# Performance work log

Hardware: AMD Instinct MI355X
Metric: run time of the kernel (lower is better)

The kernel has to match this reference:

```python
import jax, jax.numpy as jnp
import numpy as np

NEG_BIG = -9.0e15

def setup_inputs() -> dict:
    key = jax.random.key(0)
    k1, k2, k3, k4 = jax.random.split(key, 4)
    N, F_in, F_out = 2048, 512, 64
    x = jax.random.normal(k1, (N, F_in), dtype=jnp.float32)
    adj = jax.random.randint(k2, (N, N), 0, 2, dtype=jnp.int32)
    # xavier_uniform with gain=1.414
    def xavier(k, shape, gain=1.414):
        fan_in, fan_out = shape[0], shape[1]
        bound = gain * np.sqrt(6.0 / (fan_in + fan_out))
        return jax.random.uniform(k, shape, jnp.float32, -bound, bound)
    W = xavier(k3, (F_in, F_out))
    a = xavier(k4, (F_out, 1))
    return {"x": x, "adj": adj, "W": W, "a": a}

def reference(x, adj, W, a):
    h = x @ W                                  # [N, F_out]
    # pairwise |h_i - h_j| projected by a: e[i,j] = relu(sum_f |h_i,f - h_j,f| * a_f)
    diff = jnp.abs(h[:, None, :] - h[None, :, :])   # [N, N, F_out]
    e = jax.nn.relu(jnp.einsum('ijf,fo->ij', diff, a))  # [N, N]
    scores = jnp.where(adj > 0, e, NEG_BIG)
    attention = jax.nn.softmax(scores, axis=1)
    out = attention @ h                        # [N, F_out]
    return jax.nn.relu(out)                    # concat=True path
```

## Files before the change

kernel.cpp:

```cpp
#include <hip/hip_runtime.h>

#define Nn 2048
#define FIN 512
#define FO 64
#define SHIFT 20.0f
#define NJT 32
#define HS 68
#define PBS2 72
#define ZTOT (Nn * FO + Nn)

#define HX(r, f) ((r) * HS + ((((f) >> 2) ^ (((r) >> 2) & 15)) << 2))
#define HJX(r, f)  ((r) * PBS2 + ((((f) >> 3) ^ (((r) >> 2) & 7)) << 3) + ((f) & 7))
#define PX16(j, i) ((j) * PBS2 + ((((i) >> 3) ^ ((j) & 7)) << 3) + ((i) & 7))

__device__ __forceinline__ unsigned pk2(float x, float y) {
    unsigned r;
    asm("v_cvt_pk_bf16_f32 %0, %1, %2" : "=v"(r) : "v"(x), "v"(y));
    return r;
}
__device__ __forceinline__ float bflo(unsigned u) { return __uint_as_float(u << 16); }
__device__ __forceinline__ float bfhi(unsigned u) { return __uint_as_float(u & 0xffff0000u); }

__global__ __launch_bounds__(256) void gat_xw(const float* __restrict__ x,
                                              const float* __restrict__ W,
                                              float* __restrict__ h,
                                              float* __restrict__ z) {
    const int gt = blockIdx.x * 256 + threadIdx.x;
    if (z != nullptr && gt < ZTOT) z[gt] = 0.f;

    __shared__ float part[2][2][FO];
    const int wave = threadIdx.x >> 6;
    const int lane = threadIdx.x & 63;
    const int rs = wave >> 1;
    const int kh = wave & 1;
    int row = blockIdx.x * 2 + rs;
    row = __builtin_amdgcn_readfirstlane(row);
    const float* xr = x + (size_t)row * FIN + kh * (FIN / 2);
    const float* Wp = W + (size_t)kh * (FIN / 2) * FO;
    float acc = 0.f;
#pragma unroll 2
    for (int k = 0; k < FIN / 2; k += 8) {
        float4 xa = *(const float4*)(xr + k);
        float4 xb = *(const float4*)(xr + k + 4);
        acc = fmaf(xa.x, Wp[(k + 0) * FO + lane], acc);
        acc = fmaf(xa.y, Wp[(k + 1) * FO + lane], acc);
        acc = fmaf(xa.z, Wp[(k + 2) * FO + lane], acc);
        acc = fmaf(xa.w, Wp[(k + 3) * FO + lane], acc);
        acc = fmaf(xb.x, Wp[(k + 4) * FO + lane], acc);
        acc = fmaf(xb.y, Wp[(k + 5) * FO + lane], acc);
        acc = fmaf(xb.z, Wp[(k + 6) * FO + lane], acc);
        acc = fmaf(xb.w, Wp[(k + 7) * FO + lane], acc);
    }
    part[rs][kh][lane] = acc;
    __syncthreads();
    if (threadIdx.x < 128) {
        const int r2 = threadIdx.x >> 6;
        const int l2 = threadIdx.x & 63;
        h[((size_t)blockIdx.x * 2 + r2) * FO + l2] = part[r2][0][l2] + part[r2][1][l2];
    }
}

template <bool ATOMIC>
__global__ __launch_bounds__(256, 5) void gat_attn11(const float* __restrict__ h,
                                                     const int* __restrict__ adj,
                                                     const float* __restrict__ a,
                                                     float* __restrict__ po,
                                                     float* __restrict__ pl) {
    __shared__ __align__(16) float hi_s[64 * HS];
    __shared__ __align__(16) short hj16[64 * PBS2];
    __shared__ float a_s[FO];
    short* pT16 = (short*)hi_s;

    const int tid = threadIdx.x;
    const int w = tid >> 6;
    const int lane = tid & 63;
    const int li = lane & 3;
    const int lj = lane >> 2;
    const int it = blockIdx.x >> 5;
    const int jt = blockIdx.x & (NJT - 1);
    const int ib = it * 64;
    const int jb = jt * 64;
    const int iw = w * 16;

    for (int g4 = tid; g4 < 1024; g4 += 256) {
        const int row = g4 >> 4;
        const int f0 = (g4 & 15) * 4;
        *(float4*)&hi_s[HX(row, f0)] = *(const float4*)(h + (size_t)ib * FO + (size_t)g4 * 4);
        const float4 u = *(const float4*)(h + (size_t)jb * FO + (size_t)g4 * 4);
        uint2 pk;
        pk.x = pk2(u.x, u.y);
        pk.y = pk2(u.z, u.w);
        *(uint2*)&hj16[HJX(row, f0)] = pk;
    }
    if (tid < FO) a_s[tid] = a[tid];
    __syncthreads();

    float e[4][4];
#pragma unroll
    for (int di = 0; di < 4; di++)
#pragma unroll
        for (int dj = 0; dj < 4; dj++) e[di][dj] = 0.f;

#pragma unroll 4
    for (int f4 = 0; f4 < 16; f4++) {
        const float4 av = *(const float4*)&a_s[f4 * 4];
        float4 hi4[4], hj4[4];
#pragma unroll
        for (int d = 0; d < 4; d++) {
            hi4[d] = *(const float4*)&hi_s[HX(iw + 4 * li + d, f4 * 4)];
            const uint2 hw = *(const uint2*)&hj16[HJX(4 * lj + d, f4 * 4)];
            hj4[d].x = bflo(hw.x); hj4[d].y = bfhi(hw.x);
            hj4[d].z = bflo(hw.y); hj4[d].w = bfhi(hw.y);
        }
#pragma unroll
        for (int di = 0; di < 4; di++)
#pragma unroll
            for (int dj = 0; dj < 4; dj++) {
                e[di][dj] = fmaf(fabsf(hi4[di].x - hj4[dj].x), av.x, e[di][dj]);
                e[di][dj] = fmaf(fabsf(hi4[di].y - hj4[dj].y), av.y, e[di][dj]);
                e[di][dj] = fmaf(fabsf(hi4[di].z - hj4[dj].z), av.z, e[di][dj]);
                e[di][dj] = fmaf(fabsf(hi4[di].w - hj4[dj].w), av.w, e[di][dj]);
            }
    }

    float ls[4];
#pragma unroll
    for (int di = 0; di < 4; di++) ls[di] = 0.f;
#pragma unroll
    for (int di = 0; di < 4; di++) {
        const int4 am = *(const int4*)(adj + (size_t)(ib + iw + 4 * li + di) * Nn + (jb + 4 * lj));
        const int* ap = (const int*)&am;
#pragma unroll
        for (int dj = 0; dj < 4; dj++) {
            const float p = (ap[dj] > 0) ? __expf(fmaxf(e[di][dj], 0.f) - SHIFT) : 0.f;
            e[di][dj] = p;
            ls[di] += p;
        }
    }

    __syncthreads();

#pragma unroll
    for (int dj = 0; dj < 4; dj++) {
        uint2 pk;
        pk.x = pk2(e[0][dj], e[1][dj]);
        pk.y = pk2(e[2][dj], e[3][dj]);
        *(uint2*)&pT16[PX16(4 * lj + dj, iw + 4 * li)] = pk;
    }

    float pv[4][4];
#pragma unroll
    for (int u = 0; u < 4; u++)
#pragma unroll
        for (int v2 = 0; v2 < 4; v2++) pv[u][v2] = 0.f;

#pragma unroll 4
    for (int j = 0; j < 64; j++) {
        const uint2 pw = *(const uint2*)&pT16[PX16(j, iw + 4 * li)];
        const uint2 hw = *(const uint2*)&hj16[HJX(j, 4 * lj)];
        const float p0 = bflo(pw.x), p1 = bfhi(pw.x), p2 = bflo(pw.y), p3 = bfhi(pw.y);
        const float h0 = bflo(hw.x), h1 = bfhi(hw.x), h2 = bflo(hw.y), h3 = bfhi(hw.y);
        pv[0][0] = fmaf(p0, h0, pv[0][0]); pv[0][1] = fmaf(p0, h1, pv[0][1]);
        pv[0][2] = fmaf(p0, h2, pv[0][2]); pv[0][3] = fmaf(p0, h3, pv[0][3]);
        pv[1][0] = fmaf(p1, h0, pv[1][0]); pv[1][1] = fmaf(p1, h1, pv[1][1]);
        pv[1][2] = fmaf(p1, h2, pv[1][2]); pv[1][3] = fmaf(p1, h3, pv[1][3]);
        pv[2][0] = fmaf(p2, h0, pv[2][0]); pv[2][1] = fmaf(p2, h1, pv[2][1]);
        pv[2][2] = fmaf(p2, h2, pv[2][2]); pv[2][3] = fmaf(p2, h3, pv[2][3]);
        pv[3][0] = fmaf(p3, h0, pv[3][0]); pv[3][1] = fmaf(p3, h1, pv[3][1]);
        pv[3][2] = fmaf(p3, h2, pv[3][2]); pv[3][3] = fmaf(p3, h3, pv[3][3]);
    }

#pragma unroll
    for (int di = 0; di < 4; di++) {
        float v = ls[di];
        v += __shfl_xor(v, 4, 64);
        v += __shfl_xor(v, 8, 64);
        v += __shfl_xor(v, 16, 64);
        v += __shfl_xor(v, 32, 64);
        ls[di] = v;
    }

    if constexpr (!ATOMIC) {
        if (lj == 0) {
#pragma unroll
            for (int di = 0; di < 4; di++)
                pl[(size_t)jt * Nn + (ib + iw + 4 * li + di)] = ls[di];
        }
#pragma unroll
        for (int di = 0; di < 4; di++)
            *(float4*)&po[((size_t)jt * Nn + (ib + iw + 4 * li + di)) * FO + 4 * lj] =
                make_float4(pv[di][0], pv[di][1], pv[di][2], pv[di][3]);
    } else {
        if (lj == 0) {
#pragma unroll
            for (int di = 0; di < 4; di++)
                atomicAdd(&pl[ib + iw + 4 * li + di], ls[di]);
        }
#pragma unroll
        for (int di = 0; di < 4; di++) {
#pragma unroll
            for (int v2 = 0; v2 < 4; v2++)
                atomicAdd(&po[(size_t)(ib + iw + 4 * li + di) * FO + 4 * lj + v2], pv[di][v2]);
        }
    }
}

__global__ __launch_bounds__(256) void gat_reduce(const float* __restrict__ po,
                                                  const float* __restrict__ pl,
                                                  float* __restrict__ out) {
    const int t = blockIdx.x * 256 + threadIdx.x;
    const int i = t >> 6;
    float s = 0.f;
#pragma unroll
    for (int p = 0; p < NJT; p++) s += po[(size_t)p * (Nn * FO) + t];
    float l = 0.f;
#pragma unroll
    for (int p = 0; p < NJT; p++) l += pl[p * Nn + i];
    out[t] = fmaxf(s / l, 0.f);
}

__global__ __launch_bounds__(256) void gat_fin(const float* __restrict__ osum,
                                               const float* __restrict__ lsum,
                                               float* __restrict__ out) {
    const int t = blockIdx.x * 256 + threadIdx.x;
    out[t] = fmaxf(osum[t] / lsum[t >> 6], 0.f);
}

extern "C" void kernel_launch(void* const* d_in, const int* in_sizes, int n_in,
                              void* d_out, int out_size, void* d_ws, size_t ws_size,
                              hipStream_t stream) {
    const float* x   = (const float*)d_in[0];
    const int*   adj = (const int*)d_in[1];
    const float* W   = (const float*)d_in[2];
    const float* a   = (const float*)d_in[3];
    float* out = (float*)d_out;

    float* h = (float*)d_ws;
    const size_t need = ((size_t)Nn * FO + (size_t)NJT * Nn * FO + (size_t)NJT * Nn) * 4;

    if (ws_size >= need) {
        float* po = h + (size_t)Nn * FO;
        float* pl = po + (size_t)NJT * Nn * FO;
        gat_xw<<<dim3(1024), dim3(256), 0, stream>>>(x, W, h, nullptr);
        gat_attn11<false><<<dim3(32 * NJT), dim3(256), 0, stream>>>(h, adj, a, po, pl);
        gat_reduce<<<dim3(512), dim3(256), 0, stream>>>(po, pl, out);
    } else {
        float* osum = h + (size_t)Nn * FO;
        float* lsum = osum + (size_t)Nn * FO;
        gat_xw<<<dim3(1024), dim3(256), 0, stream>>>(x, W, h, osum);
        gat_attn11<true><<<dim3(32 * NJT), dim3(256), 0, stream>>>(h, adj, a, osum, lsum);
        gat_fin<<<dim3(512), dim3(256), 0, stream>>>(osum, lsum, out);
    }
}
```

Measured before the change: 121.6 us.

## Halve attention i-tile to 32 rows and raise occupancy target

The attention kernel now handles 32 query rows per block instead of 64. Each thread computes a 2x4 register tile instead of 4x4, the grid doubles to 2048 blocks, and the launch bound goes from 5 to 8 blocks per CU. Shared-memory strides and the swizzled layout for the transposed probability tile are adjusted to match. The aim is more resident waves and lower register and LDS pressure to hide latency. The cost is worse data reuse: each j-tile is loaded and converted to bf16 twice as often, and each LDS load of h_j feeds fewer FMAs.

```diff
diff --git a/kernel.cpp b/kernel.cpp
--- a/kernel.cpp
+++ b/kernel.cpp
@@ -4,14 +4,16 @@
 #define FIN 512
 #define FO 64
 #define SHIFT 20.0f
+#define NIT 64
 #define NJT 32
 #define HS 68
-#define PBS2 72
+#define HJS 68
+#define PTS3 36
 #define ZTOT (Nn * FO + Nn)
 
 #define HX(r, f) ((r) * HS + ((((f) >> 2) ^ (((r) >> 2) & 15)) << 2))
-#define HJX(r, f)  ((r) * PBS2 + ((((f) >> 3) ^ (((r) >> 2) & 7)) << 3) + ((f) & 7))
-#define PX16(j, i) ((j) * PBS2 + ((((i) >> 3) ^ ((j) & 7)) << 3) + ((i) & 7))
+#define HJX(r, f) ((r) * HJS + ((((f) >> 3) ^ (((r) >> 2) & 7)) << 3) + ((f) & 7))
+#define PXI(j, i) ((j) * PTS3 + ((((i) >> 3) ^ ((j) & 3)) << 3) + ((i) & 7))
 
 __device__ __forceinline__ unsigned pk2(float x, float y) {
     unsigned r;
@@ -61,13 +63,13 @@
 }
 
 template <bool ATOMIC>
-__global__ __launch_bounds__(256, 5) void gat_attn11(const float* __restrict__ h,
+__global__ __launch_bounds__(256, 8) void gat_attn12(const float* __restrict__ h,
                                                      const int* __restrict__ adj,
                                                      const float* __restrict__ a,
                                                      float* __restrict__ po,
                                                      float* __restrict__ pl) {
-    __shared__ __align__(16) float hi_s[64 * HS];
-    __shared__ __align__(16) short hj16[64 * PBS2];
+    __shared__ __align__(16) float hi_s[32 * HS];
+    __shared__ __align__(16) short hj16[64 * HJS];
     __shared__ float a_s[FO];
     short* pT16 = (short*)hi_s;
 
@@ -78,14 +80,19 @@
     const int lj = lane >> 2;
     const int it = blockIdx.x >> 5;
     const int jt = blockIdx.x & (NJT - 1);
-    const int ib = it * 64;
+    const int ib = it * 32;
     const int jb = jt * 64;
-    const int iw = w * 16;
-
+    const int iw = 8 * w;
+    const int i0 = iw + 2 * li;
+
+    for (int g4 = tid; g4 < 512; g4 += 256) {
+        const int row = g4 >> 4;
+        const int f0 = (g4 & 15) * 4;
+        *(float4*)&hi_s[HX(row, f0)] = *(const float4*)(h + (size_t)ib * FO + (size_t)g4 * 4);
+    }
     for (int g4 = tid; g4 < 1024; g4 += 256) {
         const int row = g4 >> 4;
         const int f0 = (g4 & 15) * 4;
-        *(float4*)&hi_s[HX(row, f0)] = *(const float4*)(h + (size_t)ib * FO + (size_t)g4 * 4);
         const float4 u = *(const float4*)(h + (size_t)jb * FO + (size_t)g4 * 4);
         uint2 pk;
         pk.x = pk2(u.x, u.y);
@@ -95,25 +102,27 @@
     if (tid < FO) a_s[tid] = a[tid];
     __syncthreads();
 
-    float e[4][4];
-#pragma unroll
-    for (int di = 0; di < 4; di++)
+    float e[2][4];
+#pragma unroll
+    for (int di = 0; di < 2; di++)
 #pragma unroll
         for (int dj = 0; dj < 4; dj++) e[di][dj] = 0.f;
 
 #pragma unroll 4
     for (int f4 = 0; f4 < 16; f4++) {
         const float4 av = *(const float4*)&a_s[f4 * 4];
-        float4 hi4[4], hj4[4];
+        float4 hi4[2], hj4[4];
+#pragma unroll
+        for (int d = 0; d < 2; d++)
+            hi4[d] = *(const float4*)&hi_s[HX(i0 + d, f4 * 4)];
 #pragma unroll
         for (int d = 0; d < 4; d++) {
-            hi4[d] = *(const float4*)&hi_s[HX(iw + 4 * li + d, f4 * 4)];
             const uint2 hw = *(const uint2*)&hj16[HJX(4 * lj + d, f4 * 4)];
             hj4[d].x = bflo(hw.x); hj4[d].y = bfhi(hw.x);
             hj4[d].z = bflo(hw.y); hj4[d].w = bfhi(hw.y);
         }
 #pragma unroll
-        for (int di = 0; di < 4; di++)
+        for (int di = 0; di < 2; di++)
 #pragma unroll
             for (int dj = 0; dj < 4; dj++) {
                 e[di][dj] = fmaf(fabsf(hi4[di].x - hj4[dj].x), av.x, e[di][dj]);
@@ -123,18 +132,16 @@
             }
     }
 
-    float ls[4];
-#pragma unroll
-    for (int di = 0; di < 4; di++) ls[di] = 0.f;
-#pragma unroll
-    for (int di = 0; di < 4; di++) {
-        const int4 am = *(const int4*)(adj + (size_t)(ib + iw + 4 * li + di) * Nn + (jb + 4 * lj));
+    float ls2[2] = {0.f, 0.f};
+#pragma unroll
+    for (int di = 0; di < 2; di++) {
+        const int4 am = *(const int4*)(adj + (size_t)(ib + i0 + di) * Nn + (jb + 4 * lj));
         const int* ap = (const int*)&am;
 #pragma unroll
         for (int dj = 0; dj < 4; dj++) {
             const float p = (ap[dj] > 0) ? __expf(fmaxf(e[di][dj], 0.f) - SHIFT) : 0.f;
             e[di][dj] = p;
-            ls[di] += p;
+            ls2[di] += p;
         }
     }
 
@@ -142,65 +149,59 @@
 
 #pragma unroll
     for (int dj = 0; dj < 4; dj++) {
-        uint2 pk;
-        pk.x = pk2(e[0][dj], e[1][dj]);
-        pk.y = pk2(e[2][dj], e[3][dj]);
-        *(uint2*)&pT16[PX16(4 * lj + dj, iw + 4 * li)] = pk;
-    }
-
-    float pv[4][4];
-#pragma unroll
-    for (int u = 0; u < 4; u++)
-#pragma unroll
-        for (int v2 = 0; v2 < 4; v2++) pv[u][v2] = 0.f;
+        const unsigned pk = pk2(e[0][dj], e[1][dj]);
+        *(unsigned*)&pT16[PXI(4 * lj + dj, i0)] = pk;
+    }
+
+    float pv[2][4];
+#pragma unroll
+    for (int di = 0; di < 2; di++)
+#pragma unroll
+        for (int c = 0; c < 4; c++) pv[di][c] = 0.f;
 
 #pragma unroll 4
     for (int j = 0; j < 64; j++) {
-        const uint2 pw = *(const uint2*)&pT16[PX16(j, iw + 4 * li)];
+        const unsigned pw = *(const unsigned*)&pT16[PXI(j, i0)];
+        const float p0 = bflo(pw), p1 = bfhi(pw);
         const uint2 hw = *(const uint2*)&hj16[HJX(j, 4 * lj)];
-        const float p0 = bflo(pw.x), p1 = bfhi(pw.x), p2 = bflo(pw.y), p3 = bfhi(pw.y);
         const float h0 = bflo(hw.x), h1 = bfhi(hw.x), h2 = bflo(hw.y), h3 = bfhi(hw.y);
         pv[0][0] = fmaf(p0, h0, pv[0][0]); pv[0][1] = fmaf(p0, h1, pv[0][1]);
         pv[0][2] = fmaf(p0, h2, pv[0][2]); pv[0][3] = fmaf(p0, h3, pv[0][3]);
         pv[1][0] = fmaf(p1, h0, pv[1][0]); pv[1][1] = fmaf(p1, h1, pv[1][1]);
         pv[1][2] = fmaf(p1, h2, pv[1][2]); pv[1][3] = fmaf(p1, h3, pv[1][3]);
-        pv[2][0] = fmaf(p2, h0, pv[2][0]); pv[2][1] = fmaf(p2, h1, pv[2][1]);
-        pv[2][2] = fmaf(p2, h2, pv[2][2]); pv[2][3] = fmaf(p2, h3, pv[2][3]);
-        pv[3][0] = fmaf(p3, h0, pv[3][0]); pv[3][1] = fmaf(p3, h1, pv[3][1]);
-        pv[3][2] = fmaf(p3, h2, pv[3][2]); pv[3][3] = fmaf(p3, h3, pv[3][3]);
-    }
-
-#pragma unroll
-    for (int di = 0; di < 4; di++) {
-        float v = ls[di];
+    }
+
+#pragma unroll
+    for (int di = 0; di < 2; di++) {
+        float v = ls2[di];
         v += __shfl_xor(v, 4, 64);
         v += __shfl_xor(v, 8, 64);
         v += __shfl_xor(v, 16, 64);
         v += __shfl_xor(v, 32, 64);
-        ls[di] = v;
+        ls2[di] = v;
     }
 
     if constexpr (!ATOMIC) {
         if (lj == 0) {
 #pragma unroll
-            for (int di = 0; di < 4; di++)
-                pl[(size_t)jt * Nn + (ib + iw + 4 * li + di)] = ls[di];
-        }
-#pragma unroll
-        for (int di = 0; di < 4; di++)
-            *(float4*)&po[((size_t)jt * Nn + (ib + iw + 4 * li + di)) * FO + 4 * lj] =
+            for (int di = 0; di < 2; di++)
+                pl[(size_t)jt * Nn + (ib + i0 + di)] = ls2[di];
+        }
+#pragma unroll
+        for (int di = 0; di < 2; di++)
+            *(float4*)&po[((size_t)jt * Nn + (ib + i0 + di)) * FO + 4 * lj] =
                 make_float4(pv[di][0], pv[di][1], pv[di][2], pv[di][3]);
     } else {
         if (lj == 0) {
 #pragma unroll
-            for (int di = 0; di < 4; di++)
-                atomicAdd(&pl[ib + iw + 4 * li + di], ls[di]);
-        }
-#pragma unroll
-        for (int di = 0; di < 4; di++) {
-#pragma unroll
-            for (int v2 = 0; v2 < 4; v2++)
-                atomicAdd(&po[(size_t)(ib + iw + 4 * li + di) * FO + 4 * lj + v2], pv[di][v2]);
+            for (int di = 0; di < 2; di++)
+                atomicAdd(&pl[ib + i0 + di], ls2[di]);
+        }
+#pragma unroll
+        for (int di = 0; di < 2; di++) {
+#pragma unroll
+            for (int c = 0; c < 4; c++)
+                atomicAdd(&po[(size_t)(ib + i0 + di) * FO + 4 * lj + c], pv[di][c]);
         }
     }
 }
@@ -242,13 +243,13 @@
         float* po = h + (size_t)Nn * FO;
         float* pl = po + (size_t)NJT * Nn * FO;
         gat_xw<<<dim3(1024), dim3(256), 0, stream>>>(x, W, h, nullptr);
-        gat_attn11<false><<<dim3(32 * NJT), dim3(256), 0, stream>>>(h, adj, a, po, pl);
+        gat_attn12<false><<<dim3(NIT * NJT), dim3(256), 0, stream>>>(h, adj, a, po, pl);
         gat_reduce<<<dim3(512), dim3(256), 0, stream>>>(po, pl, out);
     } else {
         float* osum = h + (size_t)Nn * FO;
         float* lsum = osum + (size_t)Nn * FO;
         gat_xw<<<dim3(1024), dim3(256), 0, stream>>>(x, W, h, osum);
-        gat_attn11<true><<<dim3(32 * NJT), dim3(256), 0, stream>>>(h, adj, a, osum, lsum);
+        gat_attn12<true><<<dim3(NIT * NJT), dim3(256), 0, stream>>>(h, adj, a, osum, lsum);
         gat_fin<<<dim3(512), dim3(256), 0, stream>>>(osum, lsum, out);
     }
 }
```

New measurement: 128.1 us. 5.3% more time.
